# Kernel optimization log

Measured on AMD Instinct MI355X. Metric: run time of the kernel, lower is better.

Reference implementation:

```python
import jax, jax.numpy as jnp
import numpy as np

NUM_HEADS = 8
NUM_GROUPS = 32
EPS = 1e-5


def setup_inputs() -> dict:
    key = jax.random.key(0)
    ks = jax.random.split(key, 3)
    B, C, H, W = 8, 512, 32, 32
    X = jax.random.normal(ks[0], (B, C, H, W), dtype=jnp.float32)
    norm_w = jnp.ones((C,), jnp.float32)
    norm_b = jnp.zeros((C,), jnp.float32)
    qkv_w = jax.random.normal(ks[1], (3 * C, C), dtype=jnp.float32) * (1.0 / np.sqrt(C))
    qkv_b = jnp.zeros((3 * C,), jnp.float32)
    proj_w = jax.random.normal(ks[2], (C, C), dtype=jnp.float32) * (1.0 / np.sqrt(C))
    proj_b = jnp.zeros((C,), jnp.float32)
    return {"X": X, "norm_w": norm_w, "norm_b": norm_b,
            "qkv_w": qkv_w, "qkv_b": qkv_b, "proj_w": proj_w, "proj_b": proj_b}


def group_norm(x, w, b):
    B, C, H, W = x.shape
    xg = x.reshape(B, NUM_GROUPS, C // NUM_GROUPS, H, W)
    mean = xg.mean(axis=(2, 3, 4), keepdims=True)
    var = xg.var(axis=(2, 3, 4), keepdims=True)
    xg = (xg - mean) * jax.lax.rsqrt(var + EPS)
    x = xg.reshape(B, C, H, W)
    return x * w[None, :, None, None] + b[None, :, None, None]


def reference(X, norm_w, norm_b, qkv_w, qkv_b, proj_w, proj_b):
    B, C, H, W = X.shape
    hd = C // NUM_HEADS  # head_dim
    residual = X
    Xn = group_norm(X, norm_w, norm_b)
    # 1x1 conv == channel matmul: [B, 3C, H, W]
    qkv = jnp.einsum('oc,bchw->bohw', qkv_w, Xn) + qkv_b[None, :, None, None]
    q, k, v = jnp.split(qkv, 3, axis=1)
    S = H * W
    q = q.reshape(B, NUM_HEADS, hd, S)
    k = k.reshape(B, NUM_HEADS, hd, S)
    v = v.reshape(B, NUM_HEADS, hd, S)
    scale = hd ** -0.5
    attn = jnp.einsum('bhdq,bhdk->bhqk', q, k) * scale  # [B,H,S,S]
    attn = jax.nn.softmax(attn, axis=-1)
    out = jnp.einsum('bhqk,bhdk->bhqd', attn, v)  # [B,H,S,hd]
    out = out.transpose(0, 1, 3, 2).reshape(B, C, H, W)
    out = jnp.einsum('oc,bchw->bohw', proj_w, out) + proj_b[None, :, None, None]
    return out + residual
```

## Files before the change

kernel.cpp:

```cpp
#include <hip/hip_runtime.h>
#include <hip/hip_bf16.h>


#define BATCH 8
#define C 512
#define S 1024
#define HEADS 8
#define OC3 1536

typedef short bf16x8 __attribute__((ext_vector_type(8)));
typedef float f32x4 __attribute__((ext_vector_type(4)));
typedef unsigned u32x2 __attribute__((ext_vector_type(2)));
typedef unsigned short u16;
typedef unsigned short u16x4 __attribute__((ext_vector_type(4)));

__device__ inline short f2bf(float x) {
    union { float f; unsigned u; } v; v.f = x;
    unsigned r = v.u + 0x7fffu + ((v.u >> 16) & 1u);
    return (short)(r >> 16);
}

__device__ inline unsigned cvt_pk_bf16(float lo, float hi) {
    unsigned r;
    asm("v_cvt_pk_bf16_f32 %0, %1, %2" : "=v"(r) : "v"(lo), "v"(hi));
    return r;
}

__device__ inline void gload_lds16(const u16* g, short* l) {
    __builtin_amdgcn_global_load_lds(
        (const __attribute__((address_space(1))) unsigned int*)g,
        (__attribute__((address_space(3))) unsigned int*)l, 16, 0, 0);
}

__global__ __launch_bounds__(512) void gnx_kernel(
    const float* __restrict__ X, const float* __restrict__ nw,
    const float* __restrict__ nb, u16* __restrict__ Xn_t)
{
    const int blk = blockIdx.x;
    const int bi = blk >> 5, g = blk & 31;
    const int tid = threadIdx.x;
    __shared__ __attribute__((aligned(16))) float T[16][1032];
    __shared__ float red[16];
    __shared__ float sh_mr[2];

    const float* Xg = X + ((size_t)bi * C + g * 16) * S;
    float s = 0.f, ss = 0.f;
    #pragma unroll
    for (int r = 0; r < 8; ++r) {
        int idx4 = r * 512 + tid;
        f32x4 v = *(const f32x4*)(Xg + (size_t)idx4 * 4);
        int c = idx4 >> 8, sp = (idx4 * 4) & 1023;
        *(f32x4*)&T[c][sp] = v;
        s  += v[0] + v[1] + v[2] + v[3];
        ss += v[0]*v[0] + v[1]*v[1] + v[2]*v[2] + v[3]*v[3];
    }
    #pragma unroll
    for (int m = 1; m <= 32; m <<= 1) {
        s += __shfl_xor(s, m); ss += __shfl_xor(ss, m);
    }
    if ((tid & 63) == 0) { red[tid >> 6] = s; red[8 + (tid >> 6)] = ss; }
    __syncthreads();
    if (tid == 0) {
        float S1 = 0.f, S2 = 0.f;
        #pragma unroll
        for (int w = 0; w < 8; ++w) { S1 += red[w]; S2 += red[8 + w]; }
        float mean = S1 * (1.f / 16384.f);
        float var  = S2 * (1.f / 16384.f) - mean * mean;
        sh_mr[0] = mean; sh_mr[1] = rsqrtf(var + 1e-5f);
    }
    __syncthreads();
    const float mean = sh_mr[0], rstd = sh_mr[1];
    float rw[16], sb[16];
    #pragma unroll
    for (int c = 0; c < 16; ++c) {
        float w = nw[g * 16 + c], b = nb[g * 16 + c];
        rw[c] = rstd * w;
        sb[c] = b - mean * rw[c];
    }
    #pragma unroll
    for (int r = 0; r < 2; ++r) {
        int sp = r * 512 + tid;
        bf16x8 o0, o1;
        #pragma unroll
        for (int c = 0; c < 8; ++c) o0[c] = f2bf(T[c][sp] * rw[c] + sb[c]);
        #pragma unroll
        for (int c = 0; c < 8; ++c) o1[c] = f2bf(T[8 + c][sp] * rw[8 + c] + sb[8 + c]);
        u16* dst = Xn_t + ((size_t)bi * S + sp) * C + g * 16;
        *(bf16x8*)dst = o0;
        *(bf16x8*)(dst + 8) = o1;
    }
}

__global__ __launch_bounds__(256) void wconv2(
    const float* __restrict__ wq, const float* __restrict__ wp,
    u16* __restrict__ oq, u16* __restrict__ op)
{
    int i = blockIdx.x * 256 + threadIdx.x;
    const float* w; u16* o; int j;
    if (i < 98304) { w = wq; o = oq; j = i; }
    else           { w = wp; o = op; j = i - 98304; }
    f32x4 a = *(const f32x4*)(w + (size_t)j * 8);
    f32x4 b = *(const f32x4*)(w + (size_t)j * 8 + 4);
    bf16x8 r;
    #pragma unroll
    for (int k = 0; k < 4; ++k) { r[k] = f2bf(a[k]); r[4 + k] = f2bf(b[k]); }
    *(bf16x8*)(o + (size_t)j * 8) = r;
}

__global__ __launch_bounds__(256) void qkv_mfma(
    const u16* __restrict__ A, const u16* __restrict__ Bt,
    const float* __restrict__ bias,
    u16* __restrict__ Qt, u16* __restrict__ Kt, u16* __restrict__ Vn)
{
    const int n0 = blockIdx.x * 128, m0 = blockIdx.y * 128;
    const int bi = blockIdx.z;
    const int tid = threadIdx.x, wave = tid >> 6, lane = tid & 63;
    const int lr = lane & 15, lg = lane >> 4;
    const int wr = wave >> 1, wc = wave & 1;

    __shared__ __attribute__((aligned(16))) short SM[3][8][1024];

    f32x4 acc[4][4];
    #pragma unroll
    for (int i = 0; i < 4; ++i)
        #pragma unroll
        for (int j = 0; j < 4; ++j) acc[i][j] = (f32x4){0.f, 0.f, 0.f, 0.f};

    const u16* aP0 = A + (size_t)(m0 + wave * 16 + lr) * C + lg * 8;
    const u16* aP1 = A + (size_t)(m0 + (wave + 4) * 16 + lr) * C + lg * 8;
    const u16* bP0 = Bt + (size_t)bi * S * C + (size_t)(n0 + wave * 16 + lr) * C + lg * 8;
    const u16* bP1 = Bt + (size_t)bi * S * C + (size_t)(n0 + (wave + 4) * 16 + lr) * C + lg * 8;

    auto STAGE = [&](int buf, int t) {
        const int k0 = t * 32;
        gload_lds16(aP0 + k0, &SM[buf][wave][0]);
        gload_lds16(aP1 + k0, &SM[buf][wave + 4][0]);
        gload_lds16(bP0 + k0, &SM[buf][wave][512]);
        gload_lds16(bP1 + k0, &SM[buf][wave + 4][512]);
    };

    STAGE(0, 0);
    STAGE(1, 1);
    asm volatile("s_waitcnt vmcnt(4)" ::: "memory");
    __builtin_amdgcn_s_barrier();
    __builtin_amdgcn_sched_barrier(0);

    #pragma unroll
    for (int kt = 0; kt < 16; ++kt) {
        const int cur = kt % 3;
        if (kt < 14) STAGE((kt + 2) % 3, kt + 2);
        bf16x8 af[4], bfr[4];
        #pragma unroll
        for (int mf = 0; mf < 4; ++mf) af[mf] = *(bf16x8*)&SM[cur][wr * 4 + mf][lane * 8];
        #pragma unroll
        for (int nf = 0; nf < 4; ++nf) bfr[nf] = *(bf16x8*)&SM[cur][wc * 4 + nf][512 + lane * 8];
        __builtin_amdgcn_s_setprio(1);
        #pragma unroll
        for (int mf = 0; mf < 4; ++mf)
            #pragma unroll
            for (int nf = 0; nf < 4; ++nf)
                acc[mf][nf] = __builtin_amdgcn_mfma_f32_16x16x32_bf16(
                    af[mf], bfr[nf], acc[mf][nf], 0, 0, 0);
        __builtin_amdgcn_s_setprio(0);
        if (kt < 15) {
            if (kt < 14) asm volatile("s_waitcnt vmcnt(4)" ::: "memory");
            else         asm volatile("s_waitcnt vmcnt(0)" ::: "memory");
            __builtin_amdgcn_s_barrier();
            __builtin_amdgcn_sched_barrier(0);
        }
    }

    const float QSCALE = 0.125f * 1.44269504088896f;
    if (m0 < 1024) {
        #pragma unroll
        for (int mf = 0; mf < 4; ++mf) {
            const int o3b = m0 + wr * 64 + mf * 16 + 4 * lg;
            float bv[4];
            #pragma unroll
            for (int i = 0; i < 4; ++i) bv[i] = bias[o3b + i];
            #pragma unroll
            for (int nf = 0; nf < 4; ++nf) {
                const int s = n0 + wc * 64 + nf * 16 + lr;
                if (m0 < 512) {
                    int h = o3b >> 6, d = o3b & 63;
                    u16x4 pk;
                    #pragma unroll
                    for (int i = 0; i < 4; ++i)
                        pk[i] = (u16)f2bf((acc[mf][nf][i] + bv[i]) * QSCALE);
                    *(u16x4*)(Qt + (((size_t)bi * 8 + h) * S + s) * 64 + d) = pk;
                } else {
                    int ok = o3b - 512;
                    int h = ok >> 6, d = ok & 63;
                    u16x4 pk;
                    #pragma unroll
                    for (int i = 0; i < 4; ++i) pk[i] = (u16)f2bf(acc[mf][nf][i] + bv[i]);
                    *(u16x4*)(Kt + (((size_t)bi * 8 + h) * S + s) * 64 + d) = pk;
                }
            }
        }
    } else {
        __syncthreads();
        short* Ts = &SM[0][0][0];
        #pragma unroll
        for (int mf = 0; mf < 4; ++mf) {
            const int orl = wr * 64 + mf * 16 + 4 * lg;
            float bv[4];
            #pragma unroll
            for (int i = 0; i < 4; ++i) bv[i] = bias[m0 + orl + i];
            #pragma unroll
            for (int nf = 0; nf < 4; ++nf) {
                const int srl = wc * 64 + nf * 16 + lr;
                #pragma unroll
                for (int i = 0; i < 4; ++i) {
                    int o = orl + i;
                    Ts[o * 128 + (srl ^ ((o & 7) << 3))] =
                        (short)f2bf(acc[mf][nf][i] + bv[i]);
                }
            }
        }
        __syncthreads();
        const int o = tid >> 1, half = (tid & 1) * 64;
        const int x = (o & 7) << 3;
        const int ov0 = m0 - 1024;
        u16* vdst = Vn + (size_t)(bi * C + ov0 + o) * S + n0 + half;
        #pragma unroll
        for (int c = 0; c < 8; ++c)
            *(bf16x8*)(vdst + 8 * c) = *(bf16x8*)&Ts[o * 128 + ((half + 8 * c) ^ x)];
    }
}

__global__ __launch_bounds__(512) void attn_mfma(
    const u16* __restrict__ Qt, const u16* __restrict__ Kt,
    const u16* __restrict__ Vn, u16* __restrict__ At)
{
    const int bh = blockIdx.x, qb = blockIdx.y;
    const int bi = bh >> 3, h = bh & 7;
    const int tid = threadIdx.x, wave = tid >> 6, lane = tid & 63;
    const int lr = lane & 15, lg = lane >> 4;
    const int q0 = qb * 128 + wave * 16;

    const u16* qt = Qt + ((size_t)bi * 8 + h) * S * 64;
    const u16* kp = Kt + ((size_t)bi * 8 + h) * S * 64;
    const u16* vp = Vn + (size_t)(bi * C + h * 64) * S;

    __shared__ __attribute__((aligned(16))) short Ks[2][4096];
    __shared__ __attribute__((aligned(16))) short Vs[2][4096];
    __shared__ __attribute__((aligned(16))) short Pw[8][16][64];

    bf16x8 aq0 = *(const bf16x8*)(qt + (size_t)(q0 + lr) * 64 + lg * 8);
    bf16x8 aq1 = *(const bf16x8*)(qt + (size_t)(q0 + lr) * 64 + 32 + lg * 8);

    float mrun = -1e30f, lrun = 0.f;
    f32x4 acc[4];
    #pragma unroll
    for (int df = 0; df < 4; ++df) acc[df] = (f32x4){0.f, 0.f, 0.f, 0.f};

    auto STAGE = [&](int buf, int kt0) {
        int r = tid >> 3, cs = (tid & 7) ^ (r & 7);
        short* ldsK = &Ks[buf][(wave << 6) * 8];
        short* ldsV = &Vs[buf][(wave << 6) * 8];
        gload_lds16(kp + (size_t)(kt0 + r) * 64 + cs * 8, ldsK);
        gload_lds16(vp + (size_t)r * S + kt0 + cs * 8, ldsV);
    };

    unsigned* pwb = (unsigned*)&Pw[wave][0][0];
    const int rsw = lr & 7;

    STAGE(0, 0);
    __syncthreads();

    for (int kt = 0; kt < 16; ++kt) {
        const int cur = kt & 1;
        if (kt < 15) STAGE(cur ^ 1, (kt + 1) * 64);

        f32x4 sc[4];
        __builtin_amdgcn_s_setprio(1);
        #pragma unroll
        for (int kf = 0; kf < 4; ++kf) {
            int rK = kf * 16 + lr;
            bf16x8 b0 = *(bf16x8*)&Ks[cur][rK * 64 + (lg ^ (rK & 7)) * 8];
            bf16x8 b1 = *(bf16x8*)&Ks[cur][rK * 64 + ((lg + 4) ^ (rK & 7)) * 8];
            f32x4 z = (f32x4){0.f, 0.f, 0.f, 0.f};
            z = __builtin_amdgcn_mfma_f32_16x16x32_bf16(b0, aq0, z, 0, 0, 0);
            sc[kf] = __builtin_amdgcn_mfma_f32_16x16x32_bf16(b1, aq1, z, 0, 0, 0);
        }
        __builtin_amdgcn_s_setprio(0);

        float tmax = sc[0][0];
        #pragma unroll
        for (int kf = 0; kf < 4; ++kf)
            #pragma unroll
            for (int i = 0; i < 4; ++i) tmax = fmaxf(tmax, sc[kf][i]);
        tmax = fmaxf(tmax, __shfl_xor(tmax, 16));
        tmax = fmaxf(tmax, __shfl_xor(tmax, 32));

        if (!__all(tmax <= mrun + 8.f)) {
            float mnew = fmaxf(mrun, tmax);
            float fac = __builtin_amdgcn_exp2f(mrun - mnew);
            mrun = mnew;
            lrun *= fac;
            #pragma unroll
            for (int df = 0; df < 4; ++df) acc[df] *= fac;
        }

        float sum = 0.f;
        #pragma unroll
        for (int kf = 0; kf < 4; ++kf)
            #pragma unroll
            for (int i = 0; i < 4; ++i) {
                sc[kf][i] = __builtin_amdgcn_exp2f(sc[kf][i] - mrun);
                sum += sc[kf][i];
            }

        #pragma unroll
        for (int kf = 0; kf < 4; ++kf) {
            unsigned p0 = cvt_pk_bf16(sc[kf][0], sc[kf][1]);
            unsigned p1 = cvt_pk_bf16(sc[kf][2], sc[kf][3]);
            int c0 = kf * 8 + 2 * lg;
            int idx = lr * 32 + ((c0 >> 2) ^ rsw) * 4 + (c0 & 3);
            *(u32x2*)&pwb[idx] = (u32x2){p0, p1};
        }

        sum += __shfl_xor(sum, 16);
        sum += __shfl_xor(sum, 32);
        lrun += sum;

        bf16x8 pb0 = *(bf16x8*)&Pw[wave][lr][(lg ^ rsw) * 8];
        bf16x8 pb1 = *(bf16x8*)&Pw[wave][lr][((4 + lg) ^ rsw) * 8];
        __builtin_amdgcn_s_setprio(1);
        #pragma unroll
        for (int df = 0; df < 4; ++df) {
            int rV = df * 16 + lr;
            bf16x8 v0 = *(bf16x8*)&Vs[cur][rV * 64 + (lg ^ (rV & 7)) * 8];
            bf16x8 v1 = *(bf16x8*)&Vs[cur][rV * 64 + ((lg + 4) ^ (rV & 7)) * 8];
            acc[df] = __builtin_amdgcn_mfma_f32_16x16x32_bf16(v0, pb0, acc[df], 0, 0, 0);
            acc[df] = __builtin_amdgcn_mfma_f32_16x16x32_bf16(v1, pb1, acc[df], 0, 0, 0);
        }
        __builtin_amdgcn_s_setprio(0);
        __syncthreads();
    }

    float linv = 1.f / lrun;
    #pragma unroll
    for (int df = 0; df < 4; ++df) {
        u16x4 pk;
        #pragma unroll
        for (int i = 0; i < 4; ++i) pk[i] = (u16)f2bf(acc[df][i] * linv);
        *(u16x4*)(At + ((size_t)bi * S + q0 + lr) * C + h * 64 + df * 16 + 4 * lg) = pk;
    }
}

__global__ __launch_bounds__(256) void proj_mfma(
    const u16* __restrict__ A, const u16* __restrict__ Bt,
    const float* __restrict__ bias, const float* __restrict__ Xres,
    float* __restrict__ out)
{
    const int n0 = blockIdx.x * 128, m0 = blockIdx.y * 128;
    const int bi = blockIdx.z;
    const int tid = threadIdx.x, wave = tid >> 6, lane = tid & 63;
    const int lr = lane & 15, lg = lane >> 4;
    const int wr = wave >> 1, wc = wave & 1;

    __shared__ __attribute__((aligned(16))) short SM[3][8][1024];

    f32x4 acc[4][4];
    #pragma unroll
    for (int i = 0; i < 4; ++i)
        #pragma unroll
        for (int j = 0; j < 4; ++j) acc[i][j] = (f32x4){0.f, 0.f, 0.f, 0.f};

    const u16* aP0 = A + (size_t)(m0 + wave * 16 + lr) * C + lg * 8;
    const u16* aP1 = A + (size_t)(m0 + (wave + 4) * 16 + lr) * C + lg * 8;
    const u16* bP0 = Bt + (size_t)bi * S * C + (size_t)(n0 + wave * 16 + lr) * C + lg * 8;
    const u16* bP1 = Bt + (size_t)bi * S * C + (size_t)(n0 + (wave + 4) * 16 + lr) * C + lg * 8;

    auto STAGE = [&](int buf, int t) {
        const int k0 = t * 32;
        gload_lds16(aP0 + k0, &SM[buf][wave][0]);
        gload_lds16(aP1 + k0, &SM[buf][wave + 4][0]);
        gload_lds16(bP0 + k0, &SM[buf][wave][512]);
        gload_lds16(bP1 + k0, &SM[buf][wave + 4][512]);
    };

    STAGE(0, 0);
    STAGE(1, 1);
    asm volatile("s_waitcnt vmcnt(4)" ::: "memory");
    __builtin_amdgcn_s_barrier();
    __builtin_amdgcn_sched_barrier(0);

    #pragma unroll
    for (int kt = 0; kt < 16; ++kt) {
        const int cur = kt % 3;
        if (kt < 14) STAGE((kt + 2) % 3, kt + 2);
        bf16x8 af[4], bfr[4];
        #pragma unroll
        for (int mf = 0; mf < 4; ++mf) af[mf] = *(bf16x8*)&SM[cur][wr * 4 + mf][lane * 8];
        #pragma unroll
        for (int nf = 0; nf < 4; ++nf) bfr[nf] = *(bf16x8*)&SM[cur][wc * 4 + nf][512 + lane * 8];
        __builtin_amdgcn_s_setprio(1);
        #pragma unroll
        for (int mf = 0; mf < 4; ++mf)
            #pragma unroll
            for (int nf = 0; nf < 4; ++nf)
                acc[mf][nf] = __builtin_amdgcn_mfma_f32_16x16x32_bf16(
                    af[mf], bfr[nf], acc[mf][nf], 0, 0, 0);
        __builtin_amdgcn_s_setprio(0);
        if (kt < 15) {
            if (kt < 14) asm volatile("s_waitcnt vmcnt(4)" ::: "memory");
            else         asm volatile("s_waitcnt vmcnt(0)" ::: "memory");
            __builtin_amdgcn_s_barrier();
            __builtin_amdgcn_sched_barrier(0);
        }
    }

    #pragma unroll
    for (int mf = 0; mf < 4; ++mf) {
        const int ob = m0 + wr * 64 + mf * 16 + 4 * lg;
        float bv[4];
        #pragma unroll
        for (int i = 0; i < 4; ++i) bv[i] = bias[ob + i];
        #pragma unroll
        for (int nf = 0; nf < 4; ++nf) {
            const int s = n0 + wc * 64 + nf * 16 + lr;
            #pragma unroll
            for (int i = 0; i < 4; ++i) {
                size_t oi = ((size_t)bi * C + ob + i) * S + s;
                out[oi] = acc[mf][nf][i] + bv[i] + Xres[oi];
            }
        }
    }
}

extern "C" void kernel_launch(void* const* d_in, const int* in_sizes, int n_in,
                              void* d_out, int out_size, void* d_ws, size_t ws_size,
                              hipStream_t stream) {
    const float* X      = (const float*)d_in[0];
    const float* norm_w = (const float*)d_in[1];
    const float* norm_b = (const float*)d_in[2];
    const float* qkv_w  = (const float*)d_in[3];
    const float* qkv_b  = (const float*)d_in[4];
    const float* proj_w = (const float*)d_in[5];
    const float* proj_b = (const float*)d_in[6];
    float* out = (float*)d_out;

    u16* Wq_bf = (u16*)d_ws;
    u16* Wp_bf = Wq_bf + 786432;
    u16* Xn_t  = Wp_bf + 262144;
    u16* Qt    = Xn_t + 4194304;
    u16* Kt    = Qt + 4194304;
    u16* Vn    = Kt + 4194304;
    u16* At    = Vn + 4194304;

    gnx_kernel<<<dim3(BATCH * 32), 512, 0, stream>>>(X, norm_w, norm_b, Xn_t);
    wconv2<<<dim3(512), 256, 0, stream>>>(qkv_w, proj_w, Wq_bf, Wp_bf);
    qkv_mfma<<<dim3(S / 128, OC3 / 128, BATCH), 256, 0, stream>>>(
        Wq_bf, Xn_t, qkv_b, Qt, Kt, Vn);
    attn_mfma<<<dim3(64, S / 128), 512, 0, stream>>>(Qt, Kt, Vn, At);
    proj_mfma<<<dim3(S / 128, C / 128, BATCH), 256, 0, stream>>>(
        Wp_bf, At, proj_b, X, out);
}
```

Baseline: 88.22 us.

## Give each attention wave two query tiles and fuse weight conversion into groupnorm

The attention kernel now runs 4 waves per block, each handling 32 query rows as two 16-row fragments. Every K and V fragment read from LDS then feeds twice as many MFMAs, which halves LDS traffic per FLOP but doubles accumulator and score registers per wave and halves waves per block. Separately, the bf16 weight-conversion kernel is merged into the groupnorm kernel as extra blocks, saving one kernel launch.

```diff
diff --git a/kernel.cpp b/kernel.cpp
--- a/kernel.cpp
+++ b/kernel.cpp
@@ -32,13 +32,28 @@
         (__attribute__((address_space(3))) unsigned int*)l, 16, 0, 0);
 }
 
-__global__ __launch_bounds__(512) void gnx_kernel(
+__global__ __launch_bounds__(512) void prep_kernel(
     const float* __restrict__ X, const float* __restrict__ nw,
-    const float* __restrict__ nb, u16* __restrict__ Xn_t)
+    const float* __restrict__ nb, u16* __restrict__ Xn_t,
+    const float* __restrict__ wq, const float* __restrict__ wp,
+    u16* __restrict__ oq, u16* __restrict__ op)
 {
+    const int tid = threadIdx.x;
+    if (blockIdx.x >= 256) {
+        int j = (blockIdx.x - 256) * 512 + tid;
+        const float* w; u16* o;
+        if (j < 98304) { w = wq; o = oq; }
+        else           { w = wp; o = op; j -= 98304; }
+        f32x4 a = *(const f32x4*)(w + (size_t)j * 8);
+        f32x4 b = *(const f32x4*)(w + (size_t)j * 8 + 4);
+        bf16x8 r;
+        #pragma unroll
+        for (int k = 0; k < 4; ++k) { r[k] = f2bf(a[k]); r[4 + k] = f2bf(b[k]); }
+        *(bf16x8*)(o + (size_t)j * 8) = r;
+        return;
+    }
     const int blk = blockIdx.x;
     const int bi = blk >> 5, g = blk & 31;
-    const int tid = threadIdx.x;
     __shared__ __attribute__((aligned(16))) float T[16][1032];
     __shared__ float red[16];
     __shared__ float sh_mr[2];
@@ -89,22 +104,6 @@
         *(bf16x8*)dst = o0;
         *(bf16x8*)(dst + 8) = o1;
     }
-}
-
-__global__ __launch_bounds__(256) void wconv2(
-    const float* __restrict__ wq, const float* __restrict__ wp,
-    u16* __restrict__ oq, u16* __restrict__ op)
-{
-    int i = blockIdx.x * 256 + threadIdx.x;
-    const float* w; u16* o; int j;
-    if (i < 98304) { w = wq; o = oq; j = i; }
-    else           { w = wp; o = op; j = i - 98304; }
-    f32x4 a = *(const f32x4*)(w + (size_t)j * 8);
-    f32x4 b = *(const f32x4*)(w + (size_t)j * 8 + 4);
-    bf16x8 r;
-    #pragma unroll
-    for (int k = 0; k < 4; ++k) { r[k] = f2bf(a[k]); r[4 + k] = f2bf(b[k]); }
-    *(bf16x8*)(o + (size_t)j * 8) = r;
 }
 
 __global__ __launch_bounds__(256) void qkv_mfma(
@@ -229,7 +228,7 @@
     }
 }
 
-__global__ __launch_bounds__(512) void attn_mfma(
+__global__ __launch_bounds__(256) void attn_mfma(
     const u16* __restrict__ Qt, const u16* __restrict__ Kt,
     const u16* __restrict__ Vn, u16* __restrict__ At)
 {
@@ -237,7 +236,7 @@
     const int bi = bh >> 3, h = bh & 7;
     const int tid = threadIdx.x, wave = tid >> 6, lane = tid & 63;
     const int lr = lane & 15, lg = lane >> 4;
-    const int q0 = qb * 128 + wave * 16;
+    const int q0 = qb * 128 + wave * 32;
 
     const u16* qt = Qt + ((size_t)bi * 8 + h) * S * 64;
     const u16* kp = Kt + ((size_t)bi * 8 + h) * S * 64;
@@ -245,26 +244,36 @@
 
     __shared__ __attribute__((aligned(16))) short Ks[2][4096];
     __shared__ __attribute__((aligned(16))) short Vs[2][4096];
-    __shared__ __attribute__((aligned(16))) short Pw[8][16][64];
-
-    bf16x8 aq0 = *(const bf16x8*)(qt + (size_t)(q0 + lr) * 64 + lg * 8);
-    bf16x8 aq1 = *(const bf16x8*)(qt + (size_t)(q0 + lr) * 64 + 32 + lg * 8);
-
-    float mrun = -1e30f, lrun = 0.f;
-    f32x4 acc[4];
-    #pragma unroll
-    for (int df = 0; df < 4; ++df) acc[df] = (f32x4){0.f, 0.f, 0.f, 0.f};
+    __shared__ __attribute__((aligned(16))) unsigned Pw[4][32 * 32];
+
+    bf16x8 bq[2][2];
+    #pragma unroll
+    for (int qf = 0; qf < 2; ++qf)
+        #pragma unroll
+        for (int dc = 0; dc < 2; ++dc)
+            bq[qf][dc] = *(const bf16x8*)(qt + (size_t)(q0 + qf * 16 + lr) * 64 + dc * 32 + lg * 8);
+
+    float mrun[2] = {-1e30f, -1e30f}, lrun[2] = {0.f, 0.f};
+    f32x4 acc[4][2];
+    #pragma unroll
+    for (int df = 0; df < 4; ++df)
+        #pragma unroll
+        for (int qf = 0; qf < 2; ++qf) acc[df][qf] = (f32x4){0.f, 0.f, 0.f, 0.f};
 
     auto STAGE = [&](int buf, int kt0) {
-        int r = tid >> 3, cs = (tid & 7) ^ (r & 7);
-        short* ldsK = &Ks[buf][(wave << 6) * 8];
-        short* ldsV = &Vs[buf][(wave << 6) * 8];
-        gload_lds16(kp + (size_t)(kt0 + r) * 64 + cs * 8, ldsK);
-        gload_lds16(vp + (size_t)r * S + kt0 + cs * 8, ldsV);
+        #pragma unroll
+        for (int p = 0; p < 2; ++p) {
+            int idx = p * 256 + tid;
+            int r = idx >> 3, cs = (idx & 7) ^ (r & 7);
+            short* ldsK = &Ks[buf][(p * 256 + (wave << 6)) * 8];
+            short* ldsV = &Vs[buf][(p * 256 + (wave << 6)) * 8];
+            gload_lds16(kp + (size_t)(kt0 + r) * 64 + cs * 8, ldsK);
+            gload_lds16(vp + (size_t)r * S + kt0 + cs * 8, ldsV);
+        }
     };
 
-    unsigned* pwb = (unsigned*)&Pw[wave][0][0];
-    const int rsw = lr & 7;
+    unsigned* pwb = &Pw[wave][0];
+    const int swz = (lr & 7) << 2;
 
     STAGE(0, 0);
     __syncthreads();
@@ -273,80 +282,108 @@
         const int cur = kt & 1;
         if (kt < 15) STAGE(cur ^ 1, (kt + 1) * 64);
 
-        f32x4 sc[4];
+        f32x4 sc[4][2];
         __builtin_amdgcn_s_setprio(1);
         #pragma unroll
         for (int kf = 0; kf < 4; ++kf) {
             int rK = kf * 16 + lr;
             bf16x8 b0 = *(bf16x8*)&Ks[cur][rK * 64 + (lg ^ (rK & 7)) * 8];
             bf16x8 b1 = *(bf16x8*)&Ks[cur][rK * 64 + ((lg + 4) ^ (rK & 7)) * 8];
-            f32x4 z = (f32x4){0.f, 0.f, 0.f, 0.f};
-            z = __builtin_amdgcn_mfma_f32_16x16x32_bf16(b0, aq0, z, 0, 0, 0);
-            sc[kf] = __builtin_amdgcn_mfma_f32_16x16x32_bf16(b1, aq1, z, 0, 0, 0);
+            #pragma unroll
+            for (int qf = 0; qf < 2; ++qf) {
+                f32x4 z = (f32x4){0.f, 0.f, 0.f, 0.f};
+                z = __builtin_amdgcn_mfma_f32_16x16x32_bf16(b0, bq[qf][0], z, 0, 0, 0);
+                sc[kf][qf] = __builtin_amdgcn_mfma_f32_16x16x32_bf16(b1, bq[qf][1], z, 0, 0, 0);
+            }
         }
         __builtin_amdgcn_s_setprio(0);
 
-        float tmax = sc[0][0];
+        float tmax[2];
+        #pragma unroll
+        for (int qf = 0; qf < 2; ++qf) {
+            float t = sc[0][qf][0];
+            #pragma unroll
+            for (int kf = 0; kf < 4; ++kf)
+                #pragma unroll
+                for (int i = 0; i < 4; ++i) t = fmaxf(t, sc[kf][qf][i]);
+            t = fmaxf(t, __shfl_xor(t, 16));
+            t = fmaxf(t, __shfl_xor(t, 32));
+            tmax[qf] = t;
+        }
+
+        float grow = fmaxf(tmax[0] - mrun[0], tmax[1] - mrun[1]);
+        if (!__all(grow <= 8.f)) {
+            #pragma unroll
+            for (int qf = 0; qf < 2; ++qf) {
+                float mnew = fmaxf(mrun[qf], tmax[qf]);
+                float fac = __builtin_amdgcn_exp2f(mrun[qf] - mnew);
+                mrun[qf] = mnew;
+                lrun[qf] *= fac;
+                #pragma unroll
+                for (int df = 0; df < 4; ++df) acc[df][qf] *= fac;
+            }
+        }
+
+        float sum[2] = {0.f, 0.f};
         #pragma unroll
         for (int kf = 0; kf < 4; ++kf)
             #pragma unroll
-            for (int i = 0; i < 4; ++i) tmax = fmaxf(tmax, sc[kf][i]);
-        tmax = fmaxf(tmax, __shfl_xor(tmax, 16));
-        tmax = fmaxf(tmax, __shfl_xor(tmax, 32));
-
-        if (!__all(tmax <= mrun + 8.f)) {
-            float mnew = fmaxf(mrun, tmax);
-            float fac = __builtin_amdgcn_exp2f(mrun - mnew);
-            mrun = mnew;
-            lrun *= fac;
-            #pragma unroll
-            for (int df = 0; df < 4; ++df) acc[df] *= fac;
-        }
-
-        float sum = 0.f;
+            for (int qf = 0; qf < 2; ++qf)
+                #pragma unroll
+                for (int i = 0; i < 4; ++i) {
+                    sc[kf][qf][i] = __builtin_amdgcn_exp2f(sc[kf][qf][i] - mrun[qf]);
+                    sum[qf] += sc[kf][qf][i];
+                }
+
         #pragma unroll
         for (int kf = 0; kf < 4; ++kf)
             #pragma unroll
-            for (int i = 0; i < 4; ++i) {
-                sc[kf][i] = __builtin_amdgcn_exp2f(sc[kf][i] - mrun);
-                sum += sc[kf][i];
-            }
-
-        #pragma unroll
-        for (int kf = 0; kf < 4; ++kf) {
-            unsigned p0 = cvt_pk_bf16(sc[kf][0], sc[kf][1]);
-            unsigned p1 = cvt_pk_bf16(sc[kf][2], sc[kf][3]);
-            int c0 = kf * 8 + 2 * lg;
-            int idx = lr * 32 + ((c0 >> 2) ^ rsw) * 4 + (c0 & 3);
-            *(u32x2*)&pwb[idx] = (u32x2){p0, p1};
-        }
-
-        sum += __shfl_xor(sum, 16);
-        sum += __shfl_xor(sum, 32);
-        lrun += sum;
-
-        bf16x8 pb0 = *(bf16x8*)&Pw[wave][lr][(lg ^ rsw) * 8];
-        bf16x8 pb1 = *(bf16x8*)&Pw[wave][lr][((4 + lg) ^ rsw) * 8];
+            for (int qf = 0; qf < 2; ++qf) {
+                unsigned p0 = cvt_pk_bf16(sc[kf][qf][0], sc[kf][qf][1]);
+                unsigned p1 = cvt_pk_bf16(sc[kf][qf][2], sc[kf][qf][3]);
+                int idx = (qf * 16 + lr) * 32 + ((8 * kf + 2 * lg) ^ swz);
+                *(u32x2*)&pwb[idx] = (u32x2){p0, p1};
+            }
+
+        #pragma unroll
+        for (int qf = 0; qf < 2; ++qf) {
+            sum[qf] += __shfl_xor(sum[qf], 16);
+            sum[qf] += __shfl_xor(sum[qf], 32);
+            lrun[qf] += sum[qf];
+        }
+
+        bf16x8 pb[2][2];
+        #pragma unroll
+        for (int qf = 0; qf < 2; ++qf)
+            #pragma unroll
+            for (int c = 0; c < 2; ++c)
+                pb[qf][c] = *(bf16x8*)&pwb[(qf * 16 + lr) * 32 + ((lg * 4 + 16 * c) ^ swz)];
         __builtin_amdgcn_s_setprio(1);
         #pragma unroll
         for (int df = 0; df < 4; ++df) {
             int rV = df * 16 + lr;
             bf16x8 v0 = *(bf16x8*)&Vs[cur][rV * 64 + (lg ^ (rV & 7)) * 8];
             bf16x8 v1 = *(bf16x8*)&Vs[cur][rV * 64 + ((lg + 4) ^ (rV & 7)) * 8];
-            acc[df] = __builtin_amdgcn_mfma_f32_16x16x32_bf16(v0, pb0, acc[df], 0, 0, 0);
-            acc[df] = __builtin_amdgcn_mfma_f32_16x16x32_bf16(v1, pb1, acc[df], 0, 0, 0);
+            #pragma unroll
+            for (int qf = 0; qf < 2; ++qf) {
+                acc[df][qf] = __builtin_amdgcn_mfma_f32_16x16x32_bf16(v0, pb[qf][0], acc[df][qf], 0, 0, 0);
+                acc[df][qf] = __builtin_amdgcn_mfma_f32_16x16x32_bf16(v1, pb[qf][1], acc[df][qf], 0, 0, 0);
+            }
         }
         __builtin_amdgcn_s_setprio(0);
         __syncthreads();
     }
 
-    float linv = 1.f / lrun;
-    #pragma unroll
-    for (int df = 0; df < 4; ++df) {
-        u16x4 pk;
-        #pragma unroll
-        for (int i = 0; i < 4; ++i) pk[i] = (u16)f2bf(acc[df][i] * linv);
-        *(u16x4*)(At + ((size_t)bi * S + q0 + lr) * C + h * 64 + df * 16 + 4 * lg) = pk;
+    #pragma unroll
+    for (int qf = 0; qf < 2; ++qf) {
+        float linv = 1.f / lrun[qf];
+        #pragma unroll
+        for (int df = 0; df < 4; ++df) {
+            u16x4 pk;
+            #pragma unroll
+            for (int i = 0; i < 4; ++i) pk[i] = (u16)f2bf(acc[df][qf][i] * linv);
+            *(u16x4*)(At + ((size_t)bi * S + q0 + qf * 16 + lr) * C + h * 64 + df * 16 + 4 * lg) = pk;
+        }
     }
 }
 
@@ -451,11 +488,11 @@
     u16* Vn    = Kt + 4194304;
     u16* At    = Vn + 4194304;
 
-    gnx_kernel<<<dim3(BATCH * 32), 512, 0, stream>>>(X, norm_w, norm_b, Xn_t);
-    wconv2<<<dim3(512), 256, 0, stream>>>(qkv_w, proj_w, Wq_bf, Wp_bf);
+    prep_kernel<<<dim3(512), 512, 0, stream>>>(
+        X, norm_w, norm_b, Xn_t, qkv_w, proj_w, Wq_bf, Wp_bf);
     qkv_mfma<<<dim3(S / 128, OC3 / 128, BATCH), 256, 0, stream>>>(
         Wq_bf, Xn_t, qkv_b, Qt, Kt, Vn);
-    attn_mfma<<<dim3(64, S / 128), 512, 0, stream>>>(Qt, Kt, Vn, At);
+    attn_mfma<<<dim3(64, S / 128), 256, 0, stream>>>(Qt, Kt, Vn, At);
     proj_mfma<<<dim3(S / 128, C / 128, BATCH), 256, 0, stream>>>(
         Wp_bf, At, proj_b, X, out);
 }
```

After: 88.53 us. About the same (+0.3%).
